# Optimization experiments

Hardware: AMD Instinct MI355X
Metric: run time of the kernel (lower is better)

Reference implementation:

```python
import jax, jax.numpy as jnp
import numpy as np

N_NODES = 50000
N_EDGES = 800000
IN_DIM = 64
HID = 128
OUT_DIM = 64
T_HIST = 8


def setup_inputs() -> dict:
    key = jax.random.key(0)
    ks = jax.random.split(key, 12)
    s = 0.05
    return {
        "node_feats": jax.random.normal(ks[0], (N_NODES, IN_DIM), jnp.float32),
        "history_feats": jax.random.normal(ks[1], (N_NODES, T_HIST, HID), jnp.float32),
        "src": jax.random.randint(ks[2], (N_EDGES,), 0, N_NODES, jnp.int32),
        "dst": jax.random.randint(ks[3], (N_EDGES,), 0, N_NODES, jnp.int32),
        # SAGEConv params (fc_self, fc_neigh share bias as in DGL)
        "W_self": jax.random.normal(ks[4], (IN_DIM, HID), jnp.float32) * s,
        "W_neigh": jax.random.normal(ks[5], (IN_DIM, HID), jnp.float32) * s,
        "b_sage": jnp.zeros((HID,), jnp.float32),
        # LSTM params, PyTorch gate order [i, f, g, o]
        "w_ih": jax.random.normal(ks[6], (HID, 4 * HID), jnp.float32) * s,
        "w_hh": jax.random.normal(ks[7], (HID, 4 * HID), jnp.float32) * s,
        "b_lstm": jnp.zeros((4 * HID,), jnp.float32),
        # classifier
        "W_cls": jax.random.normal(ks[8], (HID, OUT_DIM), jnp.float32) * s,
        "b_cls": jnp.zeros((OUT_DIM,), jnp.float32),
    }


def _lstm_last(x, w_ih, w_hh, b):
    # x: [N, T, H] -> last hidden state [N, H]
    N, T, H = x.shape

    def step(carry, xt):
        h, c = carry
        gates = xt @ w_ih + h @ w_hh + b  # [N, 4H]
        i, f, g, o = jnp.split(gates, 4, axis=-1)
        c = jax.nn.sigmoid(f) * c + jax.nn.sigmoid(i) * jnp.tanh(g)
        h = jax.nn.sigmoid(o) * jnp.tanh(c)
        return (h, c), None

    h0 = jnp.zeros((N, H), x.dtype)
    (h, _), _ = jax.lax.scan(step, (h0, h0), jnp.swapaxes(x, 0, 1))
    return h


def reference(node_feats, history_feats, src, dst, W_self, W_neigh, b_sage,
              w_ih, w_hh, b_lstm, W_cls, b_cls):
    N = node_feats.shape[0]
    # SAGEConv mean aggregation: mean of in-neighbor features per dst node
    msg_sum = jax.ops.segment_sum(node_feats[src], dst, num_segments=N)
    deg = jax.ops.segment_sum(jnp.ones((src.shape[0],), node_feats.dtype),
                              dst, num_segments=N)
    h_neigh = msg_sum / jnp.maximum(deg, 1.0)[:, None]
    h_struct = node_feats @ W_self + h_neigh @ W_neigh + b_sage  # [N, HID]
    # LSTM over history, take last timestep
    h_temp = _lstm_last(history_feats, w_ih, w_hh, b_lstm)  # [N, HID]
    h_combined = h_struct + h_temp
    return h_combined @ W_cls + b_cls  # [N, OUT_DIM]
```

## Files before the change

### kernel.cpp

```cpp
#include <hip/hip_runtime.h>
#include <hip/hip_bf16.h>
#include <stdint.h>

#define N_NODES 50000
#define N_EDGES 800000
#define IN_DIM 64
#define HID 128
#define OUT_DIM 64
#define T_HIST 8
#define BCAP 64

typedef __attribute__((ext_vector_type(8))) short short8;
typedef __attribute__((ext_vector_type(4))) float f32x4;

__device__ __forceinline__ unsigned short f2bf(float x) {
  unsigned int u = __builtin_bit_cast(unsigned int, x);
  unsigned int r = (u + 0x7FFFu + ((u >> 16) & 1u)) >> 16;
  return (unsigned short)r;
}
__device__ __forceinline__ short8 cvt8(float4 a, float4 b) {
  unsigned int w0, w1, w2, w3;
  asm("v_cvt_pk_bf16_f32 %0, %1, %2" : "=v"(w0) : "v"(a.x), "v"(a.y));
  asm("v_cvt_pk_bf16_f32 %0, %1, %2" : "=v"(w1) : "v"(a.z), "v"(a.w));
  asm("v_cvt_pk_bf16_f32 %0, %1, %2" : "=v"(w2) : "v"(b.x), "v"(b.y));
  asm("v_cvt_pk_bf16_f32 %0, %1, %2" : "=v"(w3) : "v"(b.z), "v"(b.w));
  struct { unsigned int a, b, c, d; } s{w0, w1, w2, w3};
  return __builtin_bit_cast(short8, s);
}
__device__ __forceinline__ float sigm(float x) {
  float e = __builtin_amdgcn_exp2f(-1.4426950408889634f * x);
  return __builtin_amdgcn_rcpf(1.f + e);
}
__device__ __forceinline__ float tanh_f(float x) {
  float e = __builtin_amdgcn_exp2f(2.8853900817779268f * x);
  return 1.f - 2.f * __builtin_amdgcn_rcpf(e + 1.f);
}

__global__ void fillpc_kernel(const int* __restrict__ src, const int* __restrict__ dst,
                              const float* __restrict__ w_ih, const float* __restrict__ w_hh,
                              const float* __restrict__ W_cls,
                              const float* __restrict__ W_self, const float* __restrict__ W_neigh,
                              const float* __restrict__ b_sage, const float* __restrict__ b_cls,
                              unsigned short* __restrict__ Wt2, unsigned short* __restrict__ Wc2,
                              float* __restrict__ Wsc, float* __restrict__ Wnc,
                              float* __restrict__ bc1,
                              int* __restrict__ cnt, int* __restrict__ esrc) {
  int tid = blockIdx.x * blockDim.x + threadIdx.x;
  int stride = gridDim.x * blockDim.x;
  for (int e = tid; e < N_EDGES; e += stride) {
    int d = dst[e];
    int pos = atomicAdd(&cnt[d], 1);
    if (pos < BCAP) esrc[d * BCAP + pos] = src[e];
  }
  for (int idx = tid; idx < 256 * 512; idx += stride) {
    int i = idx & 7;
    int lane = (idx >> 3) & 63;
    int F = idx >> 9;
    int q = F >> 5, g = (F >> 3) & 3, kk = F & 7;
    int c = g * 128 + q * 16 + (lane & 15);
    int k = kk * 32 + (lane >> 4) * 8 + i;
    float v = (k < 128) ? w_ih[k * 512 + c] : w_hh[(k - 128) * 512 + c];
    Wt2[idx] = f2bf(v);
  }
  for (int idx = tid; idx < 16 * 512; idx += stride) {
    int i = idx & 7;
    int lane = (idx >> 3) & 63;
    int F = idx >> 9;
    int cb = F >> 2, kk = F & 3;
    int col = cb * 16 + (lane & 15);
    int k = kk * 32 + (lane >> 4) * 8 + i;
    Wc2[idx] = f2bf(W_cls[k * 64 + col]);
  }
  for (int idx = tid; idx < 64 * 64; idx += stride) {
    int k = idx >> 6, c = idx & 63;
    float as = 0.f, an = 0.f;
    for (int m = 0; m < 128; m++) {
      float wc = W_cls[m * 64 + c];
      as += W_self[k * 128 + m] * wc;
      an += W_neigh[k * 128 + m] * wc;
    }
    Wsc[idx] = as;
    Wnc[idx] = an;
  }
  for (int c = tid; c < 64; c += stride) {
    float acc = b_cls[c];
    for (int m = 0; m < 128; m++) acc += b_sage[m] * W_cls[m * 64 + c];
    bc1[c] = acc;
  }
}

#define HS_TILE 32
__global__ __launch_bounds__(512) void hstruct_kernel(
    const float* __restrict__ nf, const int* __restrict__ esrc,
    const int* __restrict__ cnt,
    const float* __restrict__ Wsc, const float* __restrict__ Wnc, const float* __restrict__ bc1,
    float* __restrict__ out1) {
  __shared__ float s_nf[HS_TILE][IN_DIM + 1];
  __shared__ float s_hn[HS_TILE][IN_DIM + 1];
  int tid = threadIdx.x;
  int node0 = blockIdx.x * HS_TILE;
  for (int i = tid; i < HS_TILE * IN_DIM; i += 512) {
    int r = i >> 6, k = i & 63;
    int node = node0 + r;
    s_nf[r][k] = (node < N_NODES) ? nf[node * 64 + k] : 0.f;
  }
  int wv = tid >> 6, lane = tid & 63;
  for (int r = wv; r < HS_TILE; r += 8) {
    int node = node0 + r;
    float a0 = 0.f, a1 = 0.f, a2 = 0.f, a3 = 0.f;
    int n = 0;
    if (node < N_NODES) {
      n = cnt[node];
      int nl = (n < BCAP) ? n : BCAP;
      int st = node * BCAP;
      int j = 0;
      for (; j + 4 <= nl; j += 4) {
        int s0 = esrc[st + j], s1 = esrc[st + j + 1];
        int s2 = esrc[st + j + 2], s3 = esrc[st + j + 3];
        a0 += nf[s0 * 64 + lane];
        a1 += nf[s1 * 64 + lane];
        a2 += nf[s2 * 64 + lane];
        a3 += nf[s3 * 64 + lane];
      }
      for (; j < nl; j++) a0 += nf[esrc[st + j] * 64 + lane];
    }
    s_hn[r][lane] = (a0 + a1 + a2 + a3) * __builtin_amdgcn_rcpf(fmaxf((float)n, 1.f));
  }
  __syncthreads();
  int r = tid & 31;
  int c0 = (tid >> 5) * 4;
  float accs[4] = {0.f, 0.f, 0.f, 0.f};
  for (int k = 0; k < IN_DIM; k++) {
    float a = s_nf[r][k];
    float b = s_hn[r][k];
    float4 w1 = *(const float4*)&Wsc[k * 64 + c0];
    float4 w2 = *(const float4*)&Wnc[k * 64 + c0];
    accs[0] += a * w1.x + b * w2.x;
    accs[1] += a * w1.y + b * w2.y;
    accs[2] += a * w1.z + b * w2.z;
    accs[3] += a * w1.w + b * w2.w;
  }
  int node = node0 + r;
  if (node < N_NODES) {
    #pragma unroll
    for (int i = 0; i < 4; i++)
      out1[(size_t)node * 64 + c0 + i] = accs[i] + bc1[c0 + i];
  }
}

#define LB 32
__global__ __launch_bounds__(512, 2) void lstm_kernel(
    const float* __restrict__ hist,
    const unsigned short* __restrict__ Wt2,
    const unsigned short* __restrict__ Wc2,
    const float* __restrict__ b_lstm,
    const float* __restrict__ out1,
    float* __restrict__ out)
{
  __shared__ alignas(16) unsigned short Abuf[2][LB * 256];

  const int tid = threadIdx.x;
  const int lane = tid & 63;
  const int w = tid >> 6;
  const int l15 = lane & 15;
  const int l4 = lane >> 4;
  const int base = blockIdx.x * LB;
  const int jj = w * 16 + l15;

  short8 Bfr[4][8];
  #pragma unroll
  for (int g = 0; g < 4; g++)
    #pragma unroll
    for (int kk = 0; kk < 8; kk++)
      Bfr[g][kk] = *(const short8*)&Wt2[((w * 32 + g * 8 + kk) * 64 + lane) * 8];

  const float bi  = b_lstm[jj];
  const float bf_ = b_lstm[128 + jj];
  const float bg  = b_lstm[256 + jj];
  const float bo  = b_lstm[384 + jj];

  float c_st[8];
  #pragma unroll
  for (int i = 0; i < 8; i++) c_st[i] = 0.f;

  {
    int row = tid >> 4;
    int kb = tid & 15;
    short8 z = {0,0,0,0,0,0,0,0};
    *(short8*)&Abuf[0][row * 256 + 128 + kb * 8] = z;
    int node = base + row;
    float4 x0 = make_float4(0.f,0.f,0.f,0.f), x1 = make_float4(0.f,0.f,0.f,0.f);
    if (node < N_NODES) {
      const float4* p = (const float4*)&hist[(size_t)node * (T_HIST * HID) + kb * 8];
      x0 = p[0]; x1 = p[1];
    }
    int sb = (kb & 8) | ((kb & 7) ^ (row & 7));
    *(short8*)&Abuf[0][row * 256 + sb * 8] = cvt8(x0, x1);
  }
  __syncthreads();

  float4 xpa, xpb;
  const int srow = tid >> 4, skb = tid & 15;

  #pragma unroll
  for (int t = 0; t < T_HIST - 1; t++) {
    unsigned short* Acur = &Abuf[t & 1][0];
    unsigned short* Anxt = &Abuf[(t & 1) ^ 1][0];

    {
      int node = base + srow;
      if (node < N_NODES) {
        const float4* p = (const float4*)&hist[(size_t)node * (T_HIST * HID) + (t + 1) * HID + skb * 8];
        xpa = p[0]; xpb = p[1];
      } else {
        xpa = make_float4(0.f,0.f,0.f,0.f);
        xpb = make_float4(0.f,0.f,0.f,0.f);
      }
    }

    #pragma unroll
    for (int rb = 0; rb < 2; rb++) {
      f32x4 acc[4];
      #pragma unroll
      for (int g = 0; g < 4; g++) { f32x4 z = {0.f,0.f,0.f,0.f}; acc[g] = z; }
      #pragma unroll
      for (int kk = 0; kk < 8; kk++) {
        int row = rb * 16 + l15;
        int kb = kk * 4 + l4;
        int sb = (kb & 24) | ((kb & 7) ^ (row & 7));
        short8 a = *(const short8*)&Acur[row * 256 + sb * 8];
        #pragma unroll
        for (int g = 0; g < 4; g++)
          acc[g] = __builtin_amdgcn_mfma_f32_16x16x32_bf16(a, Bfr[g][kk], acc[g], 0, 0, 0);
      }
      #pragma unroll
      for (int reg = 0; reg < 4; reg++) {
        int r = rb * 4 + reg;
        float gi = sigm(acc[0][reg] + bi);
        float gf = sigm(acc[1][reg] + bf_);
        float gg = tanh_f(acc[2][reg] + bg);
        float go = sigm(acc[3][reg] + bo);
        float c = gf * c_st[r] + gi * gg;
        c_st[r] = c;
        float h = go * tanh_f(c);
        int row = rb * 16 + l4 * 4 + reg;
        int kb = 16 + (jj >> 3);
        int sb = (kb & 24) | ((kb & 7) ^ (row & 7));
        Anxt[row * 256 + sb * 8 + (jj & 7)] = f2bf(h);
      }
    }

    {
      int sb = (skb & 8) | ((skb & 7) ^ (srow & 7));
      *(short8*)&Anxt[srow * 256 + sb * 8] = cvt8(xpa, xpb);
    }
    __syncthreads();
  }

  {
    unsigned short* Acur = &Abuf[1][0];
    unsigned short* Anxt = &Abuf[0][0];

    #pragma unroll
    for (int rb = 0; rb < 2; rb++) {
      f32x4 acc[4];
      #pragma unroll
      for (int g = 0; g < 4; g++) { f32x4 z = {0.f,0.f,0.f,0.f}; acc[g] = z; }
      #pragma unroll
      for (int kk = 0; kk < 8; kk++) {
        int row = rb * 16 + l15;
        int kb = kk * 4 + l4;
        int sb = (kb & 24) | ((kb & 7) ^ (row & 7));
        short8 a = *(const short8*)&Acur[row * 256 + sb * 8];
        #pragma unroll
        for (int g = 0; g < 4; g++)
          acc[g] = __builtin_amdgcn_mfma_f32_16x16x32_bf16(a, Bfr[g][kk], acc[g], 0, 0, 0);
      }
      #pragma unroll
      for (int reg = 0; reg < 4; reg++) {
        int r = rb * 4 + reg;
        float gi = sigm(acc[0][reg] + bi);
        float gf = sigm(acc[1][reg] + bf_);
        float gg = tanh_f(acc[2][reg] + bg);
        float go = sigm(acc[3][reg] + bo);
        float c = gf * c_st[r] + gi * gg;
        float h = go * tanh_f(c);
        int row = rb * 16 + l4 * 4 + reg;
        int kb = jj >> 3;
        int sb = (kb & 8) | ((kb & 7) ^ (row & 7));
        Anxt[row * 256 + sb * 8 + (jj & 7)] = f2bf(h);
      }
    }
    __syncthreads();

    {
      int rbo = w >> 2, cbo = w & 3;
      int col = cbo * 16 + l15;
      float ov[4];
      #pragma unroll
      for (int reg = 0; reg < 4; reg++) {
        int row = rbo * 16 + l4 * 4 + reg;
        int node = base + row;
        ov[reg] = (node < N_NODES) ? out1[(size_t)node * OUT_DIM + col] : 0.f;
      }
      f32x4 o = {0.f, 0.f, 0.f, 0.f};
      #pragma unroll
      for (int kk = 0; kk < 4; kk++) {
        short8 bv = *(const short8*)&Wc2[((cbo * 4 + kk) * 64 + lane) * 8];
        int row = rbo * 16 + l15;
        int kb = kk * 4 + l4;
        int sb = (kb & 8) | ((kb & 7) ^ (row & 7));
        short8 a = *(const short8*)&Anxt[row * 256 + sb * 8];
        o = __builtin_amdgcn_mfma_f32_16x16x32_bf16(a, bv, o, 0, 0, 0);
      }
      #pragma unroll
      for (int reg = 0; reg < 4; reg++) {
        int row = rbo * 16 + l4 * 4 + reg;
        int node = base + row;
        if (node < N_NODES) out[(size_t)node * OUT_DIM + col] = o[reg] + ov[reg];
      }
    }
  }
}

extern "C" void kernel_launch(void* const* d_in, const int* in_sizes, int n_in,
                              void* d_out, int out_size, void* d_ws, size_t ws_size,
                              hipStream_t stream) {
  (void)in_sizes; (void)n_in; (void)out_size; (void)ws_size;
  const float* node_feats = (const float*)d_in[0];
  const float* hist       = (const float*)d_in[1];
  const int*   src        = (const int*)d_in[2];
  const int*   dst        = (const int*)d_in[3];
  const float* W_self     = (const float*)d_in[4];
  const float* W_neigh    = (const float*)d_in[5];
  const float* b_sage     = (const float*)d_in[6];
  const float* w_ih       = (const float*)d_in[7];
  const float* w_hh       = (const float*)d_in[8];
  const float* b_lstm     = (const float*)d_in[9];
  const float* W_cls      = (const float*)d_in[10];
  const float* b_cls      = (const float*)d_in[11];
  float* out = (float*)d_out;

  char* ws = (char*)d_ws;
  int* cnt        = (int*)(ws);
  int* esrc       = (int*)(ws + 200192);
  float* out1     = (float*)(ws + 13000192);
  unsigned short* Wt2 = (unsigned short*)(ws + 25800192);
  unsigned short* Wc2 = (unsigned short*)(ws + 26062336);
  float* Wsc      = (float*)(ws + 26078720);
  float* Wnc      = (float*)(ws + 26095104);
  float* bc1      = (float*)(ws + 26111488);

  hipMemsetAsync(cnt, 0, N_NODES * sizeof(int), stream);
  fillpc_kernel<<<(N_EDGES + 255) / 256, 256, 0, stream>>>(
      src, dst, w_ih, w_hh, W_cls, W_self, W_neigh, b_sage, b_cls,
      Wt2, Wc2, Wsc, Wnc, bc1, cnt, esrc);
  hstruct_kernel<<<(N_NODES + HS_TILE - 1) / HS_TILE, 512, 0, stream>>>(
      node_feats, esrc, cnt, Wsc, Wnc, bc1, out1);
  lstm_kernel<<<(N_NODES + LB - 1) / LB, 512, 0, stream>>>(
      hist, Wt2, Wc2, b_lstm, out1, out);
}
```

Baseline: 307.7 us.

## Double LSTM block tile to 64 nodes per workgroup and add sched barriers

```diff
diff --git a/kernel.cpp b/kernel.cpp
--- a/kernel.cpp
+++ b/kernel.cpp
@@ -148,7 +148,7 @@
   }
 }
 
-#define LB 32
+#define LB 64
 __global__ __launch_bounds__(512, 2) void lstm_kernel(
     const float* __restrict__ hist,
     const unsigned short* __restrict__ Wt2,
@@ -157,7 +157,7 @@
     const float* __restrict__ out1,
     float* __restrict__ out)
 {
-  __shared__ alignas(16) unsigned short Abuf[2][LB * 256];
+  __shared__ alignas(16) unsigned short Abuf[2][64 * 256];
 
   const int tid = threadIdx.x;
   const int lane = tid & 63;
@@ -179,15 +179,21 @@
   const float bg  = b_lstm[256 + jj];
   const float bo  = b_lstm[384 + jj];
 
-  float c_st[8];
+  float c_st[16];
   #pragma unroll
-  for (int i = 0; i < 8; i++) c_st[i] = 0.f;
-
-  {
-    int row = tid >> 4;
-    int kb = tid & 15;
+  for (int i = 0; i < 16; i++) c_st[i] = 0.f;
+
+  for (int u = tid; u < 64 * 16; u += 512) {
+    int row = u >> 4;
+    int kbh = u & 15;
     short8 z = {0,0,0,0,0,0,0,0};
-    *(short8*)&Abuf[0][row * 256 + 128 + kb * 8] = z;
+    *(short8*)&Abuf[0][row * 256 + 128 + kbh * 8] = z;
+  }
+  #pragma unroll
+  for (int i2 = 0; i2 < 2; i2++) {
+    int u = tid + (i2 << 9);
+    int row = u >> 4;
+    int kb = u & 15;
     int node = base + row;
     float4 x0 = make_float4(0.f,0.f,0.f,0.f), x1 = make_float4(0.f,0.f,0.f,0.f);
     if (node < N_NODES) {
@@ -199,27 +205,31 @@
   }
   __syncthreads();
 
-  float4 xpa, xpb;
-  const int srow = tid >> 4, skb = tid & 15;
+  float4 xp[4];
 
   #pragma unroll
   for (int t = 0; t < T_HIST - 1; t++) {
     unsigned short* Acur = &Abuf[t & 1][0];
     unsigned short* Anxt = &Abuf[(t & 1) ^ 1][0];
 
-    {
-      int node = base + srow;
+    #pragma unroll
+    for (int i2 = 0; i2 < 2; i2++) {
+      int u = tid + (i2 << 9);
+      int row = u >> 4;
+      int kb = u & 15;
+      int node = base + row;
       if (node < N_NODES) {
-        const float4* p = (const float4*)&hist[(size_t)node * (T_HIST * HID) + (t + 1) * HID + skb * 8];
-        xpa = p[0]; xpb = p[1];
+        const float4* p = (const float4*)&hist[(size_t)node * (T_HIST * HID) + (t + 1) * HID + kb * 8];
+        xp[i2 * 2]     = p[0];
+        xp[i2 * 2 + 1] = p[1];
       } else {
-        xpa = make_float4(0.f,0.f,0.f,0.f);
-        xpb = make_float4(0.f,0.f,0.f,0.f);
-      }
-    }
-
-    #pragma unroll
-    for (int rb = 0; rb < 2; rb++) {
+        xp[i2 * 2]     = make_float4(0.f,0.f,0.f,0.f);
+        xp[i2 * 2 + 1] = make_float4(0.f,0.f,0.f,0.f);
+      }
+    }
+
+    #pragma unroll
+    for (int rb = 0; rb < 4; rb++) {
       f32x4 acc[4];
       #pragma unroll
       for (int g = 0; g < 4; g++) { f32x4 z = {0.f,0.f,0.f,0.f}; acc[g] = z; }
@@ -248,11 +258,16 @@
         int sb = (kb & 24) | ((kb & 7) ^ (row & 7));
         Anxt[row * 256 + sb * 8 + (jj & 7)] = f2bf(h);
       }
-    }
-
-    {
-      int sb = (skb & 8) | ((skb & 7) ^ (srow & 7));
-      *(short8*)&Anxt[srow * 256 + sb * 8] = cvt8(xpa, xpb);
+      __builtin_amdgcn_sched_barrier(0);
+    }
+
+    #pragma unroll
+    for (int i2 = 0; i2 < 2; i2++) {
+      int u = tid + (i2 << 9);
+      int row = u >> 4;
+      int kb = u & 15;
+      int sb = (kb & 8) | ((kb & 7) ^ (row & 7));
+      *(short8*)&Anxt[row * 256 + sb * 8] = cvt8(xp[i2 * 2], xp[i2 * 2 + 1]);
     }
     __syncthreads();
   }
@@ -262,7 +277,7 @@
     unsigned short* Anxt = &Abuf[0][0];
 
     #pragma unroll
-    for (int rb = 0; rb < 2; rb++) {
+    for (int rb = 0; rb < 4; rb++) {
       f32x4 acc[4];
       #pragma unroll
       for (int g = 0; g < 4; g++) { f32x4 z = {0.f,0.f,0.f,0.f}; acc[g] = z; }
@@ -290,11 +305,14 @@
         int sb = (kb & 8) | ((kb & 7) ^ (row & 7));
         Anxt[row * 256 + sb * 8 + (jj & 7)] = f2bf(h);
       }
+      __builtin_amdgcn_sched_barrier(0);
     }
     __syncthreads();
 
-    {
-      int rbo = w >> 2, cbo = w & 3;
+    #pragma unroll
+    for (int fi = 0; fi < 2; fi++) {
+      int f = w * 2 + fi;
+      int rbo = f >> 2, cbo = f & 3;
       int col = cbo * 16 + l15;
       float ov[4];
       #pragma unroll
```

Result: no change. 308.0 us (median of 2 runs) (+0.1%).
